# Kernel optimization log

Measured on AMD Instinct MI355X. Metric: run time of the kernel, lower is better.

## Reference

```python
import jax, jax.numpy as jnp
import numpy as np

B, N, D = 64, 8192, 128
REPLACE = 0.0  # stands in for torch.inf default; kept finite for numerics


def setup_inputs() -> dict:
    key = jax.random.key(0)
    k1, k2 = jax.random.split(key)
    X = jax.random.normal(k1, (B, N, D), dtype=jnp.float32)
    # mask True == position masked OUT (module computes ~mask to get valid)
    mask = jax.random.randint(k2, (B, N), 0, 2) == 1
    W = jnp.ones((D,), dtype=jnp.float32)
    b = jnp.zeros((D,), dtype=jnp.float32)
    return {"X": X, "mask": mask, "W": W, "b": b}


def reference(X, mask, W, b):
    # valid positions: ~mask, broadcast across feature dim
    valid = (~mask)[:, :, None].astype(X.dtype)          # [B, N, 1]
    count = jnp.sum(valid, axis=1)                       # [B, 1]
    mean = jnp.sum(X * valid, axis=1) / count            # [B, D]
    centered = X - mean[:, None, :]                      # [B, N, D]
    # torch masked std is unbiased (ddof=1)
    var = jnp.sum((centered * centered) * valid, axis=1) / (count - 1.0)
    std = jnp.sqrt(var)                                  # [B, D]
    normed = centered / std[:, None, :]                  # [B, N, D]
    # diag_embed(W) + F.linear == elementwise affine
    out = normed * W + b
    # masked positions were filled with REPLACE before the affine step
    out = jnp.where(mask[:, :, None], REPLACE * W + b, out)
    return out
```

## Files before the change

kernel.cpp:

```cpp
#include <hip/hip_runtime.h>

#define B_ 64
#define N_ 8192
#define D_ 128
#define D4 (D_ / 4)
#define NCHUNKS 16
#define CHUNK (N_ / NCHUNKS)

#define WS_SUM    0
#define WS_SUMSQ  (B_ * D_)
#define WS_COUNT  (2 * B_ * D_)
#define WS_SCALE  (2 * B_ * D_ + B_)
#define WS_SHIFT  (3 * B_ * D_ + B_)
#define WS_ZERO_N (2 * B_ * D_ + B_)

__global__ __launch_bounds__(256) void init_ws(float* __restrict__ ws) {
    int i = blockIdx.x * blockDim.x + threadIdx.x;
    if (i < WS_ZERO_N) ws[i] = 0.0f;
}

__global__ __launch_bounds__(256) void reduce_kernel(
        const float* __restrict__ X, const int* __restrict__ mask,
        float* __restrict__ ws) {
    float* __restrict__ sum   = ws + WS_SUM;
    float* __restrict__ sumsq = ws + WS_SUMSQ;
    float* __restrict__ count = ws + WS_COUNT;

    const int b   = blockIdx.x;
    const int n0  = blockIdx.y * CHUNK;
    const int tid = threadIdx.x;
    const int q   = tid & 31;
    const int sub = tid >> 5;

    const float4* __restrict__ Xr = (const float4*)(X + (size_t)b * N_ * D_);
    const int*    __restrict__ mr = mask + b * N_;

    float4 s  = make_float4(0.f, 0.f, 0.f, 0.f);
    float4 ss = make_float4(0.f, 0.f, 0.f, 0.f);
    float  cnt = 0.f;

    for (int n = n0 + sub; n < n0 + CHUNK; n += 8) {
        if (mr[n] == 0) {
            float4 x = Xr[(size_t)n * D4 + q];
            s.x += x.x;  s.y += x.y;  s.z += x.z;  s.w += x.w;
            ss.x += x.x * x.x;  ss.y += x.y * x.y;
            ss.z += x.z * x.z;  ss.w += x.w * x.w;
            if (q == 0) cnt += 1.f;
        }
    }

    __shared__ float4 sh_s[8][32];
    __shared__ float4 sh_ss[8][32];
    __shared__ float  sh_c[8];
    sh_s[sub][q]  = s;
    sh_ss[sub][q] = ss;
    if (q == 0) sh_c[sub] = cnt;
    __syncthreads();

    if (sub == 0) {
        float4 ts = s, tss = ss;
        for (int k = 1; k < 8; ++k) {
            float4 a = sh_s[k][q], bb = sh_ss[k][q];
            ts.x += a.x;  ts.y += a.y;  ts.z += a.z;  ts.w += a.w;
            tss.x += bb.x; tss.y += bb.y; tss.z += bb.z; tss.w += bb.w;
        }
        const int base = b * D_ + q * 4;
        atomicAdd(&sum[base + 0], ts.x);
        atomicAdd(&sum[base + 1], ts.y);
        atomicAdd(&sum[base + 2], ts.z);
        atomicAdd(&sum[base + 3], ts.w);
        atomicAdd(&sumsq[base + 0], tss.x);
        atomicAdd(&sumsq[base + 1], tss.y);
        atomicAdd(&sumsq[base + 2], tss.z);
        atomicAdd(&sumsq[base + 3], tss.w);
    }
    if (tid == 0) {
        float c = 0.f;
        for (int k = 0; k < 8; ++k) c += sh_c[k];
        atomicAdd(&count[b], c);
    }
}

__global__ __launch_bounds__(256) void finalize_kernel(
        const float* __restrict__ W, const float* __restrict__ bias,
        float* __restrict__ ws) {
    const float* __restrict__ sum   = ws + WS_SUM;
    const float* __restrict__ sumsq = ws + WS_SUMSQ;
    const float* __restrict__ count = ws + WS_COUNT;
    float* __restrict__ scale = ws + WS_SCALE;
    float* __restrict__ shift = ws + WS_SHIFT;

    int i = blockIdx.x * blockDim.x + threadIdx.x;
    if (i >= B_ * D_) return;
    int b = i >> 7;
    int d = i & (D_ - 1);
    float c    = count[b];
    float s    = sum[i];
    float sq   = sumsq[i];
    float mean = s / c;
    float var  = (sq - s * mean) / (c - 1.0f);
    float inv  = rsqrtf(var);
    float sc   = W[d] * inv;
    scale[i] = sc;
    shift[i] = bias[d] - mean * sc;
}

__global__ __launch_bounds__(256) void normalize_kernel(
        const float* __restrict__ X, const int* __restrict__ mask,
        const float* __restrict__ ws, const float* __restrict__ bias,
        float* __restrict__ out) {
    const float4* __restrict__ X4 = (const float4*)X;
    float4* __restrict__ O4 = (float4*)out;
    const float4* __restrict__ S4 = (const float4*)(ws + WS_SCALE);
    const float4* __restrict__ H4 = (const float4*)(ws + WS_SHIFT);
    const float4* __restrict__ B4 = (const float4*)bias;

    const long long total = (long long)B_ * N_ * D4;
    long long i = (long long)blockIdx.x * blockDim.x + threadIdx.x;
    const long long stride = (long long)gridDim.x * blockDim.x;

    for (; i < total; i += stride) {
        int row = (int)(i >> 5);
        int c   = (int)(i & 31);
        int b   = row >> 13;
        float4 o;
        if (mask[row] != 0) {
            o = B4[c];
        } else {
            float4 x  = X4[i];
            float4 sc = S4[b * D4 + c];
            float4 sh = H4[b * D4 + c];
            o.x = x.x * sc.x + sh.x;
            o.y = x.y * sc.y + sh.y;
            o.z = x.z * sc.z + sh.z;
            o.w = x.w * sc.w + sh.w;
        }
        O4[i] = o;
    }
}

extern "C" void kernel_launch(void* const* d_in, const int* in_sizes, int n_in,
                              void* d_out, int out_size, void* d_ws, size_t ws_size,
                              hipStream_t stream) {
    const float* X    = (const float*)d_in[0];
    const int*   mask = (const int*)d_in[1];
    const float* W    = (const float*)d_in[2];
    const float* bias = (const float*)d_in[3];
    float* out = (float*)d_out;
    float* ws  = (float*)d_ws;

    init_ws<<<(WS_ZERO_N + 255) / 256, 256, 0, stream>>>(ws);

    reduce_kernel<<<dim3(B_, NCHUNKS), 256, 0, stream>>>(X, mask, ws);

    finalize_kernel<<<(B_ * D_ + 255) / 256, 256, 0, stream>>>(W, bias, ws);

    normalize_kernel<<<4096, 256, 0, stream>>>(X, mask, ws, bias, out);
}
```

Baseline: 491.7 us.

## Replace atomics with per-chunk partials, branchless loads, and nontemporal output stores

The reduction now writes per-chunk partial sums and counts to distinct workspace slots, and the finalize kernel sums them. This removes the init kernel launch and the float atomics. Both the reduce and normalize loops now load X unconditionally and select with the mask instead of branching, so memory accesses are uniform and can be unrolled. Output uses nontemporal stores to avoid cache pollution. The trade-off is that X rows for masked positions, about half of them, are now read even though they are not needed.

```diff
diff --git a/kernel.cpp b/kernel.cpp
--- a/kernel.cpp
+++ b/kernel.cpp
@@ -7,100 +7,93 @@
 #define NCHUNKS 16
 #define CHUNK (N_ / NCHUNKS)
 
-#define WS_SUM    0
-#define WS_SUMSQ  (B_ * D_)
-#define WS_COUNT  (2 * B_ * D_)
-#define WS_SCALE  (2 * B_ * D_ + B_)
-#define WS_SHIFT  (3 * B_ * D_ + B_)
-#define WS_ZERO_N (2 * B_ * D_ + B_)
+typedef float v4f __attribute__((ext_vector_type(4)));
 
-__global__ __launch_bounds__(256) void init_ws(float* __restrict__ ws) {
-    int i = blockIdx.x * blockDim.x + threadIdx.x;
-    if (i < WS_ZERO_N) ws[i] = 0.0f;
-}
+#define WS_SUMP  0
+#define WS_SQP   (B_ * NCHUNKS * D_)
+#define WS_CNTP  (2 * B_ * NCHUNKS * D_)
+#define WS_SCALE (2 * B_ * NCHUNKS * D_ + B_ * NCHUNKS)
+#define WS_SHIFT (WS_SCALE + B_ * D_)
 
 __global__ __launch_bounds__(256) void reduce_kernel(
         const float* __restrict__ X, const int* __restrict__ mask,
         float* __restrict__ ws) {
-    float* __restrict__ sum   = ws + WS_SUM;
-    float* __restrict__ sumsq = ws + WS_SUMSQ;
-    float* __restrict__ count = ws + WS_COUNT;
-
     const int b   = blockIdx.x;
-    const int n0  = blockIdx.y * CHUNK;
+    const int cy  = blockIdx.y;
     const int tid = threadIdx.x;
     const int q   = tid & 31;
     const int sub = tid >> 5;
+    const int n0  = cy * CHUNK;
 
-    const float4* __restrict__ Xr = (const float4*)(X + (size_t)b * N_ * D_);
-    const int*    __restrict__ mr = mask + b * N_;
+    const v4f* __restrict__ Xr = (const v4f*)(X + (size_t)b * N_ * D_);
+    const int* __restrict__ mr = mask + b * N_;
 
-    float4 s  = make_float4(0.f, 0.f, 0.f, 0.f);
-    float4 ss = make_float4(0.f, 0.f, 0.f, 0.f);
-    float  cnt = 0.f;
+    v4f s  = (v4f)(0.f);
+    v4f ss = (v4f)(0.f);
+    float cnt = 0.f;
 
-    for (int n = n0 + sub; n < n0 + CHUNK; n += 8) {
-        if (mr[n] == 0) {
-            float4 x = Xr[(size_t)n * D4 + q];
-            s.x += x.x;  s.y += x.y;  s.z += x.z;  s.w += x.w;
-            ss.x += x.x * x.x;  ss.y += x.y * x.y;
-            ss.z += x.z * x.z;  ss.w += x.w * x.w;
-            if (q == 0) cnt += 1.f;
-        }
+    #pragma unroll 4
+    for (int k = 0; k < CHUNK / 8; ++k) {
+        const int n = n0 + sub + 8 * k;
+        const float v = (mr[n] == 0) ? 1.0f : 0.0f;
+        v4f x = Xr[(size_t)n * D4 + q];
+        x *= v;
+        s += x;
+        ss += x * x;
+        cnt += v;
     }
 
-    __shared__ float4 sh_s[8][32];
-    __shared__ float4 sh_ss[8][32];
-    __shared__ float  sh_c[8];
+    __shared__ v4f sh_s[8][32];
+    __shared__ v4f sh_ss[8][32];
+    __shared__ float sh_c[8];
     sh_s[sub][q]  = s;
     sh_ss[sub][q] = ss;
     if (q == 0) sh_c[sub] = cnt;
     __syncthreads();
 
     if (sub == 0) {
-        float4 ts = s, tss = ss;
+        v4f ts = s, tss = ss;
         for (int k = 1; k < 8; ++k) {
-            float4 a = sh_s[k][q], bb = sh_ss[k][q];
-            ts.x += a.x;  ts.y += a.y;  ts.z += a.z;  ts.w += a.w;
-            tss.x += bb.x; tss.y += bb.y; tss.z += bb.z; tss.w += bb.w;
+            ts  += sh_s[k][q];
+            tss += sh_ss[k][q];
         }
-        const int base = b * D_ + q * 4;
-        atomicAdd(&sum[base + 0], ts.x);
-        atomicAdd(&sum[base + 1], ts.y);
-        atomicAdd(&sum[base + 2], ts.z);
-        atomicAdd(&sum[base + 3], ts.w);
-        atomicAdd(&sumsq[base + 0], tss.x);
-        atomicAdd(&sumsq[base + 1], tss.y);
-        atomicAdd(&sumsq[base + 2], tss.z);
-        atomicAdd(&sumsq[base + 3], tss.w);
+        v4f* __restrict__ sump = (v4f*)(ws + WS_SUMP);
+        v4f* __restrict__ sqp  = (v4f*)(ws + WS_SQP);
+        const int slot = (b * NCHUNKS + cy) * D4 + q;
+        sump[slot] = ts;
+        sqp[slot]  = tss;
     }
     if (tid == 0) {
         float c = 0.f;
         for (int k = 0; k < 8; ++k) c += sh_c[k];
-        atomicAdd(&count[b], c);
+        ws[WS_CNTP + b * NCHUNKS + cy] = c;
     }
 }
 
 __global__ __launch_bounds__(256) void finalize_kernel(
         const float* __restrict__ W, const float* __restrict__ bias,
         float* __restrict__ ws) {
-    const float* __restrict__ sum   = ws + WS_SUM;
-    const float* __restrict__ sumsq = ws + WS_SUMSQ;
-    const float* __restrict__ count = ws + WS_COUNT;
+    const float* __restrict__ sump = ws + WS_SUMP;
+    const float* __restrict__ sqp  = ws + WS_SQP;
+    const float* __restrict__ cntp = ws + WS_CNTP;
     float* __restrict__ scale = ws + WS_SCALE;
     float* __restrict__ shift = ws + WS_SHIFT;
 
-    int i = blockIdx.x * blockDim.x + threadIdx.x;
+    const int i = blockIdx.x * blockDim.x + threadIdx.x;
     if (i >= B_ * D_) return;
-    int b = i >> 7;
-    int d = i & (D_ - 1);
-    float c    = count[b];
-    float s    = sum[i];
-    float sq   = sumsq[i];
-    float mean = s / c;
-    float var  = (sq - s * mean) / (c - 1.0f);
-    float inv  = rsqrtf(var);
-    float sc   = W[d] * inv;
+    const int b = i >> 7;
+    const int d = i & (D_ - 1);
+
+    float c = 0.f, s = 0.f, sq = 0.f;
+    #pragma unroll
+    for (int cy = 0; cy < NCHUNKS; ++cy) {
+        c  += cntp[b * NCHUNKS + cy];
+        s  += sump[(b * NCHUNKS + cy) * D_ + d];
+        sq += sqp [(b * NCHUNKS + cy) * D_ + d];
+    }
+    const float mean = s / c;
+    const float var  = (sq - s * mean) / (c - 1.0f);
+    const float sc   = W[d] * rsqrtf(var);
     scale[i] = sc;
     shift[i] = bias[d] - mean * sc;
 }
@@ -109,33 +102,32 @@
         const float* __restrict__ X, const int* __restrict__ mask,
         const float* __restrict__ ws, const float* __restrict__ bias,
         float* __restrict__ out) {
-    const float4* __restrict__ X4 = (const float4*)X;
-    float4* __restrict__ O4 = (float4*)out;
-    const float4* __restrict__ S4 = (const float4*)(ws + WS_SCALE);
-    const float4* __restrict__ H4 = (const float4*)(ws + WS_SHIFT);
-    const float4* __restrict__ B4 = (const float4*)bias;
+    const v4f* __restrict__ X4 = (const v4f*)X;
+    v4f* __restrict__ O4 = (v4f*)out;
+    const v4f* __restrict__ S4 = (const v4f*)(ws + WS_SCALE);
+    const v4f* __restrict__ H4 = (const v4f*)(ws + WS_SHIFT);
+    const v4f* __restrict__ B4 = (const v4f*)bias;
 
     const long long total = (long long)B_ * N_ * D4;
     long long i = (long long)blockIdx.x * blockDim.x + threadIdx.x;
     const long long stride = (long long)gridDim.x * blockDim.x;
 
     for (; i < total; i += stride) {
-        int row = (int)(i >> 5);
-        int c   = (int)(i & 31);
-        int b   = row >> 13;
-        float4 o;
-        if (mask[row] != 0) {
-            o = B4[c];
-        } else {
-            float4 x  = X4[i];
-            float4 sc = S4[b * D4 + c];
-            float4 sh = H4[b * D4 + c];
-            o.x = x.x * sc.x + sh.x;
-            o.y = x.y * sc.y + sh.y;
-            o.z = x.z * sc.z + sh.z;
-            o.w = x.w * sc.w + sh.w;
-        }
-        O4[i] = o;
+        const int row = (int)(i >> 5);
+        const int c   = (int)(i & 31);
+        const int b   = row >> 13;
+        const int m   = mask[row];
+        const v4f x  = X4[i];
+        const v4f sc = S4[b * D4 + c];
+        const v4f sh = H4[b * D4 + c];
+        const v4f bb = B4[c];
+        const v4f norm = x * sc + sh;
+        v4f o;
+        o.x = m ? bb.x : norm.x;
+        o.y = m ? bb.y : norm.y;
+        o.z = m ? bb.z : norm.z;
+        o.w = m ? bb.w : norm.w;
+        __builtin_nontemporal_store(o, &O4[i]);
     }
 }
 
@@ -149,8 +141,6 @@
     float* out = (float*)d_out;
     float* ws  = (float*)d_ws;
 
-    init_ws<<<(WS_ZERO_N + 255) / 256, 256, 0, stream>>>(ws);
-
     reduce_kernel<<<dim3(B_, NCHUNKS), 256, 0, stream>>>(X, mask, ws);
 
     finalize_kernel<<<(B_ * D_ + 255) / 256, 256, 0, stream>>>(W, bias, ws);
```

Result: no change. 493.3 us (+0.3%).
